# Kernel optimization log

Hardware: AMD Instinct MI355X
Metric: run time of the kernel (lower is better)

Reference implementation:

```python
import jax, jax.numpy as jnp
import numpy as np

NS, BS, U, NR, NT, D = 256, 7, 8, 4, 8, 2
ITERS, HID = 3, 200
P, NOISE = 100.0, 1e-7
CIN = 2 * NT * D  # block input width: flattened Z1 and Z2


def setup_inputs() -> dict:
    key = jax.random.key(0)
    ks = jax.random.split(key, 21)
    rn = lambda k, s: jax.random.normal(k, s, dtype=jnp.float32)
    inp = {
        'H_re': rn(ks[0], (NS, BS, BS, U, NR, NT)),
        'H_im': rn(ks[1], (NS, BS, BS, U, NR, NT)),
        'V_re': rn(ks[2], (NS, BS, U, NT, D)),
        'V_im': rn(ks[3], (NS, BS, U, NT, D)),
        'w': jnp.ones((U,), jnp.float32),
        'W1_re': rn(ks[4], (ITERS, HID, CIN)) * 0.05,
        'W1_im': rn(ks[5], (ITERS, HID, CIN)) * 0.05,
        'b1_re': rn(ks[6], (ITERS, HID)) * 0.05,
        'b1_im': rn(ks[7], (ITERS, HID)) * 0.05,
        'W2_re': rn(ks[8], (ITERS, HID, HID)) * 0.05,
        'W2_im': rn(ks[9], (ITERS, HID, HID)) * 0.05,
        'b2_re': rn(ks[10], (ITERS, HID)) * 0.05,
        'b2_im': rn(ks[11], (ITERS, HID)) * 0.05,
        'W3_re': rn(ks[12], (ITERS, HID, HID)) * 0.05,
        'W3_im': rn(ks[13], (ITERS, HID, HID)) * 0.05,
        'b3_re': rn(ks[14], (ITERS, HID)) * 0.05,
        'b3_im': rn(ks[15], (ITERS, HID)) * 0.05,
        'W4_re': rn(ks[16], (ITERS, 1, HID)) * 0.05,
        'W4_im': rn(ks[17], (ITERS, 1, HID)) * 0.05,
        'b4_re': rn(ks[18], (ITERS, 1)) * 0.05,
        'b4_im': rn(ks[19], (ITERS, 1)) * 0.05,
    }
    return inp


def _crelu(x):
    # ComplexReLU: relu on real part, imaginary part passes through
    return jax.nn.relu(x.real) + 1j * x.imag


def _clin(x, W, b):
    # torch Linear with complex weights: x @ W.T + b
    return jnp.einsum('...i,oi->...o', x, W) + b


def _iteration(H, V, w, p):
    n = H.shape[0]
    Z = V
    # HV[n,k,l,i,j] = H[n,k,l,i] @ V[n,k,j]  -> [n,BS,BS,U,U,NR,D]
    HV = jnp.einsum('nklirt,nkjtd->nklijrd', H, V)
    ab = jnp.arange(BS)
    au = jnp.arange(U)
    HV2 = HV[:, ab, ab][:, :, au, au]  # HV[:,k,k,i,i] -> [n,BS,U,NR,D]
    # T[n,k,l,i,j] = HV @ HV^H -> [n,BS,BS,U,U,NR,NR]
    T = jnp.einsum('nklijrd,nklijsd->nklijrs', HV, HV.conj())
    I_r = jnp.eye(NR, dtype=HV.dtype)
    # U[n,l,u] = noise*I + sum_{k,j} T[n,k,l,u,j]
    Usum = NOISE * I_r + T.sum(axis=(1, 4))  # [n,BS,U,NR,NR]
    Y = jnp.linalg.solve(Usum, HV2)
    Td = T[:, ab, ab][:, :, au, au]  # T[:,l,l,u,u]
    F = Usum - Td
    Gamma = jnp.einsum('nlurd,nlure->nlude', HV2.conj(), jnp.linalg.solve(F, HV2))
    IG = jnp.eye(D, dtype=HV.dtype) + Gamma  # [n,BS,U,D,D]
    # A[n,l,m,u] = H[n,l,m,u].mH @ Y[n,m,u] -> [n,BS,BS,U,NT,D]
    A = jnp.einsum('nlmurt,nmurd->nlmutd', H.conj(), Y)
    # L[n,l,u] = sum_m A @ IG[m,u] @ A^H -> [n,BS,U,NT,NT]
    L = jnp.einsum('nlmutd,nmude,nlmuse->nluts', A, IG, A.conj())
    All = A[:, ab, ab]  # A[:,l,l] -> [n,BS,U,NT,D]
    Lam = jnp.einsum('nlutd,nlude->nlute', All, IG)
    wv = w.astype(HV.dtype)[None, None, :, None, None]
    Lam = Lam * wv
    L = L * wv
    Z2 = Lam - jnp.einsum('nluts,nlusd->nlutd', L, Z)
    inp = jnp.concatenate([Z.reshape(n, BS, U, NT * D), Z2.reshape(n, BS, U, NT * D)], -1)
    W1, b1, W2, b2, W3, b3, W4, b4 = p
    h = _crelu(_clin(inp, W1, b1))
    h = _crelu(_clin(h, W2, b2))
    h = _crelu(_clin(h, W3, b3))
    step = _clin(h, W4, b4).real  # [n,BS,U,1]
    Vn = Z + step[..., None] * Z2
    fro = (jnp.abs(Vn) ** 2).sum((-2, -1)).sum(2)  # [n,BS]
    scale = jnp.where(fro > P, jnp.sqrt(P / fro), 1.0)
    return Vn * scale[:, :, None, None, None].astype(Vn.dtype)


def reference(H_re, H_im, V_re, V_im, w, W1_re, W1_im, b1_re, b1_im, W2_re, W2_im, b2_re, b2_im, W3_re, W3_im, b3_re, b3_im, W4_re, W4_im, b4_re, b4_im):
    H = (H_re + 1j * H_im).astype(jnp.complex64)
    V = (V_re + 1j * V_im).astype(jnp.complex64)
    # init_input power normalization per (sample, BS)
    fro0 = (jnp.abs(V) ** 2).sum((-2, -1)).sum(2)
    V = V * jnp.sqrt(P / fro0)[:, :, None, None, None].astype(V.dtype)
    c64 = jnp.complex64
    Ws = [(W1_re + 1j * W1_im).astype(c64), (b1_re + 1j * b1_im).astype(c64),
          (W2_re + 1j * W2_im).astype(c64), (b2_re + 1j * b2_im).astype(c64),
          (W3_re + 1j * W3_im).astype(c64), (b3_re + 1j * b3_im).astype(c64),
          (W4_re + 1j * W4_im).astype(c64), (b4_re + 1j * b4_im).astype(c64)]
    for it in range(ITERS):
        p = tuple(a[it] for a in Ws)
        V = _iteration(H, V, w, p)
    return jnp.stack([V.real, V.imag], axis=-1)
```

## Files before the change

kernel.cpp:

```cpp
#include <hip/hip_runtime.h>
#include <math.h>

#define NS 256
#define BS 7
#define UU 8
#define NR 4
#define NT 8
#define DD 2
#define HID 200
#define CIN 32
#define PP 100.0f
#define NOISEF 1e-7f

typedef _Float16 f16x8 __attribute__((ext_vector_type(8)));
typedef float f32x4 __attribute__((ext_vector_type(4)));

#define AST 424
#define AST0 104
#define NTILES 28
#define B1_KC 3
#define B23_KC 13
#define B1_HALVES (B1_KC*NTILES*64*8)
#define B23_HALVES (B23_KC*NTILES*64*8)
#define BITER_HALVES (B1_HALVES + 2*B23_HALVES)
#define MROWS 32

__device__ void chol_solve(const float2 (*A)[NR], const float2 (*B)[DD], float2 (*X)[DD]) {
  float2 L[NR][NR];
  for (int j = 0; j < NR; ++j) {
    float d = A[j][j].x;
    for (int k = 0; k < j; ++k) d -= L[j][k].x * L[j][k].x + L[j][k].y * L[j][k].y;
    float ld = sqrtf(fmaxf(d, 1e-30f));
    L[j][j] = make_float2(ld, 0.f);
    float inv = 1.f / ld;
    for (int i = j + 1; i < NR; ++i) {
      float sr = A[i][j].x, si = A[i][j].y;
      for (int k = 0; k < j; ++k) {
        float2 a = L[i][k], b = L[j][k];
        sr -= a.x * b.x + a.y * b.y;
        si -= a.y * b.x - a.x * b.y;
      }
      L[i][j] = make_float2(sr * inv, si * inv);
    }
  }
  for (int c = 0; c < DD; ++c) {
    float2 z[NR];
    for (int i = 0; i < NR; ++i) {
      float sr = B[i][c].x, si = B[i][c].y;
      for (int k = 0; k < i; ++k) {
        float2 a = L[i][k], zz = z[k];
        sr -= a.x * zz.x - a.y * zz.y;
        si -= a.x * zz.y + a.y * zz.x;
      }
      float inv = 1.f / L[i][i].x;
      z[i] = make_float2(sr * inv, si * inv);
    }
    for (int i = NR - 1; i >= 0; --i) {
      float sr = z[i].x, si = z[i].y;
      for (int k = i + 1; k < NR; ++k) {
        float2 a = L[k][i], xx = X[k][c];
        sr -= a.x * xx.x + a.y * xx.y;
        si -= a.x * xx.y - a.y * xx.x;
      }
      float inv = 1.f / L[i][i].x;
      X[i][c] = make_float2(sr * inv, si * inv);
    }
  }
}

__global__ void k_norm0(const float* __restrict__ Vre, const float* __restrict__ Vim,
                        float2* __restrict__ Vcur) {
  int nl = blockIdx.x;
  int tid = threadIdx.x;
  size_t base = (size_t)nl * 128;
  float re = Vre[base + tid], im = Vim[base + tid];
  float p = re * re + im * im;
  p += __shfl_down(p, 32); p += __shfl_down(p, 16); p += __shfl_down(p, 8);
  p += __shfl_down(p, 4);  p += __shfl_down(p, 2);  p += __shfl_down(p, 1);
  __shared__ float sred[2];
  if ((tid & 63) == 0) sred[tid >> 6] = p;
  __syncthreads();
  float fro = sred[0] + sred[1];
  float sc = sqrtf(PP / fro);
  Vcur[base + tid] = make_float2(re * sc, im * sc);
}

__global__ __launch_bounds__(512, 2) void k_s1n(const float* __restrict__ Hre,
    const float* __restrict__ Him, const float2* __restrict__ Vcur,
    float2* __restrict__ Yb, float2* __restrict__ IGb) {
  int n = blockIdx.x;
  int tid = threadIdx.x;
  int wave = tid >> 6;
  int lane = tid & 63;
  int i = lane >> 3, c = lane & 7;

  __shared__ float2 Vs[952];
  __shared__ float2 Cs[7][76];
  __shared__ float2 Hl[7][268];
  __shared__ float2 Gk[7][8][10];
  __shared__ float2 Gs[56][10];
  __shared__ float2 TdL[56][10];
  __shared__ float2 HV2L[56][8];

  const float2* Vn = Vcur + (size_t)n * 896;
  for (int idx = tid; idx < 896; idx += 512)
    Vs[(idx >> 4) * 17 + (idx & 15)] = Vn[idx];
  __syncthreads();

  if (tid < 448) {
    int k = tid >> 6, e = tid & 63, cc = e >> 3, t = e & 7;
    float sr = 0.f, si = 0.f;
    #pragma unroll
    for (int j = 0; j < 8; ++j) {
      const float2* vr = &Vs[(k * 8 + j) * 17];
      #pragma unroll
      for (int d = 0; d < 2; ++d) {
        float2 a = vr[t * 2 + d], b = vr[cc * 2 + d];
        sr += a.x * b.x + a.y * b.y;
        si += a.y * b.x - a.x * b.y;
      }
    }
    Cs[k][cc * 9 + t] = make_float2(sr, si);
  }

  for (int l = 0; l < BS; ++l) {
    __syncthreads();
    if (tid < 448) {
      int k = tid >> 6;
      int e4 = (tid & 63) * 4;
      size_t hbase = (((size_t)(n * 7 + k) * 7) + l) * 256 + e4;
      float4 re = *(const float4*)(Hre + hbase);
      float4 im = *(const float4*)(Him + hbase);
      int ii = e4 >> 5, rem = e4 & 31;
      float2* hp = &Hl[k][ii * 33 + rem];
      hp[0] = make_float2(re.x, im.x);
      hp[1] = make_float2(re.y, im.y);
      hp[2] = make_float2(re.z, im.z);
      hp[3] = make_float2(re.w, im.w);
    }
    __syncthreads();

    if (wave < 7) {
      int k = wave;
      const float2* hme = &Hl[k][i * 33];
      const float2* cme = &Cs[k][c * 9];
      float2 T[4];
      #pragma unroll
      for (int r = 0; r < 4; ++r) {
        float tr = 0.f, ti = 0.f;
        #pragma unroll
        for (int t = 0; t < 8; ++t) {
          float2 h = hme[r * 8 + t], cv = cme[t];
          tr += h.x * cv.x - h.y * cv.y;
          ti += h.x * cv.y + h.y * cv.x;
        }
        T[r] = make_float2(tr, ti);
      }
      float2 hb[4];
      #pragma unroll
      for (int s = 0; s < 4; ++s) hb[s] = hme[s * 8 + c];
      float2 G[10];
      {
        int ui = 0;
        #pragma unroll
        for (int r = 0; r < 4; ++r)
          #pragma unroll
          for (int s = r; s < 4; ++s) {
            G[ui].x = T[r].x * hb[s].x + T[r].y * hb[s].y;
            G[ui].y = T[r].y * hb[s].x - T[r].x * hb[s].y;
            ++ui;
          }
      }
      #pragma unroll
      for (int m = 1; m < 8; m <<= 1) {
        #pragma unroll
        for (int q = 0; q < 10; ++q) {
          G[q].x += __shfl_xor(G[q].x, m);
          G[q].y += __shfl_xor(G[q].y, m);
        }
      }
      if (c == 0) {
        #pragma unroll
        for (int q = 0; q < 10; ++q) Gk[k][i][q] = G[q];
      }

      if (k == l) {
        int r = c >> 1, d = c & 1;
        float hvx = 0.f, hvy = 0.f;
        const float2* vp = &Vs[(l * 8 + i) * 17 + d];
        #pragma unroll
        for (int t = 0; t < 8; ++t) {
          float2 h = hme[r * 8 + t], v = vp[t * 2];
          hvx += h.x * v.x - h.y * v.y;
          hvy += h.x * v.y + h.y * v.x;
        }
        float gx[8], gy[8];
        int base = lane & 56;
        #pragma unroll
        for (int p = 0; p < 8; ++p) {
          gx[p] = __shfl(hvx, base + p);
          gy[p] = __shfl(hvy, base + p);
        }
        if (c == 0) {
          int ui = 0;
          #pragma unroll
          for (int r2 = 0; r2 < 4; ++r2)
            #pragma unroll
            for (int s2 = r2; s2 < 4; ++s2) {
              float tr = 0.f, ti = 0.f;
              #pragma unroll
              for (int d2 = 0; d2 < 2; ++d2) {
                float ax = gx[r2 * 2 + d2], ay = gy[r2 * 2 + d2];
                float bx = gx[s2 * 2 + d2], by = gy[s2 * 2 + d2];
                tr += ax * bx + ay * by;
                ti += ay * bx - ax * by;
              }
              TdL[l * 8 + i][ui] = make_float2(tr, ti);
              ++ui;
            }
          #pragma unroll
          for (int x = 0; x < 8; ++x)
            HV2L[l * 8 + i][x] = make_float2(gx[x], gy[x]);
        }
      }
    }
    __syncthreads();
    if (tid < 80) {
      int ii = tid / 10, q = tid % 10;
      float sx = 0.f, sy = 0.f;
      #pragma unroll
      for (int k = 0; k < 7; ++k) {
        float2 g = Gk[k][ii][q];
        sx += g.x; sy += g.y;
      }
      Gs[l * 8 + ii][q] = make_float2(sx, sy);
    }
  }
  __syncthreads();

  if (tid < 128) {
    int which = tid >> 6;
    int b = tid & 63;
    if (b < 56) {
      float2 M[NR][NR];
      int ui = 0;
      #pragma unroll
      for (int r = 0; r < 4; ++r)
        #pragma unroll
        for (int s = r; s < 4; ++s) {
          float2 g = Gs[b][ui];
          if (which) { float2 td = TdL[b][ui]; g.x -= td.x; g.y -= td.y; }
          ++ui;
          M[r][s] = g;
          M[s][r] = make_float2(g.x, -g.y);
        }
      #pragma unroll
      for (int r = 0; r < 4; ++r) { M[r][r].x += NOISEF; M[r][r].y = 0.f; }
      float2 Bv[NR][DD], X[NR][DD];
      #pragma unroll
      for (int x = 0; x < 8; ++x) Bv[x >> 1][x & 1] = HV2L[b][x];
      chol_solve(M, Bv, X);
      size_t gb = (size_t)n * 56 + b;
      if (!which) {
        #pragma unroll
        for (int x = 0; x < 8; ++x) Yb[gb * 8 + x] = X[x >> 1][x & 1];
      } else {
        #pragma unroll
        for (int d = 0; d < DD; ++d)
          #pragma unroll
          for (int e = 0; e < DD; ++e) {
            float gr = (d == e) ? 1.f : 0.f, gi = 0.f;
            #pragma unroll
            for (int r = 0; r < NR; ++r) {
              float2 a = Bv[r][d], x = X[r][e];
              gr += a.x * x.x + a.y * x.y;
              gi += a.x * x.y - a.y * x.x;
            }
            IGb[gb * 4 + d * 2 + e] = make_float2(gr, gi);
          }
      }
    }
  }
}

__global__ __launch_bounds__(256) void k_stage2(const float* __restrict__ Hre,
    const float* __restrict__ Him, const float2* __restrict__ Vcur,
    const float2* __restrict__ Yb, const float2* __restrict__ IGb,
    const float* __restrict__ w, float2* __restrict__ Z2out) {
  int nl = blockIdx.x; int l = nl % BS; int n = nl / BS;
  int tid = threadIdx.x;
  __shared__ float2 SM[3686];
  float2* Hsm  = SM;
  float2* Bsm  = SM;
  float2* Lsm  = SM + 952;
  float2* Ysm  = SM + 1792;
  float2* IGsm = SM + 2247;
  float2* Asm  = SM + 2478;
  float2* Lamm = SM + 3430;
  float2* Zlm  = SM + 3558;

  size_t hbase = ((size_t)n * BS + l) * 1792;
  for (int idx = tid; idx < 1792; idx += 256) {
    int t = idx & 7, r = (idx >> 3) & 3, u = (idx >> 5) & 7, m = idx >> 8;
    Hsm[((u * 4 + r) * 7 + m) * 8 + t] = make_float2(Hre[hbase + idx], Him[hbase + idx]);
  }
  const float2* yp = Yb + (size_t)n * 448;
  for (int idx = tid; idx < 448; idx += 256)
    Ysm[(idx >> 6) * 65 + (idx & 63)] = yp[idx];
  const float2* igp = IGb + (size_t)n * 224;
  if (tid < 224) IGsm[(tid >> 5) * 33 + (tid & 31)] = igp[tid];
  const float2* zp = Vcur + (size_t)nl * 128;
  if (tid < 128) Zlm[tid] = zp[tid];
  __syncthreads();

  for (int idx = tid; idx < 896; idx += 256) {
    int u = idx / 112, rem = idx % 112, m = rem >> 4, t = (rem >> 1) & 7, d = rem & 1;
    float ar = 0.f, ai = 0.f;
    #pragma unroll
    for (int r = 0; r < NR; ++r) {
      float2 h = Hsm[((u * 4 + r) * 7 + m) * 8 + t];
      float2 y = Ysm[m * 65 + u * 8 + r * 2 + d];
      ar += h.x * y.x + h.y * y.y;
      ai += h.x * y.y - h.y * y.x;
    }
    Asm[u * 119 + m * 17 + t * 2 + d] = make_float2(ar, ai);
  }
  __syncthreads();

  for (int idx = tid; idx < 896; idx += 256) {
    int u = idx / 112, rem = idx % 112, m = rem >> 4, t = (rem >> 1) & 7, e = rem & 1;
    float br = 0.f, bi = 0.f;
    #pragma unroll
    for (int d = 0; d < DD; ++d) {
      float2 a = Asm[u * 119 + m * 17 + t * 2 + d];
      float2 g = IGsm[m * 33 + u * 4 + d * 2 + e];
      br += a.x * g.x - a.y * g.y;
      bi += a.x * g.y + a.y * g.x;
    }
    Bsm[u * 119 + m * 17 + t * 2 + e] = make_float2(br, bi);
  }
  __syncthreads();

  for (int idx = tid; idx < 512; idx += 256) {
    int u = idx >> 6, t = (idx >> 3) & 7, s = idx & 7;
    float lr = 0.f, li = 0.f;
    #pragma unroll
    for (int m = 0; m < BS; ++m)
      #pragma unroll
      for (int e = 0; e < DD; ++e) {
        float2 bb = Bsm[u * 119 + m * 17 + t * 2 + e];
        float2 ac = Asm[u * 119 + m * 17 + s * 2 + e];
        lr += bb.x * ac.x + bb.y * ac.y;
        li += bb.y * ac.x - bb.x * ac.y;
      }
    float wu = w[u];
    Lsm[(u * 8 + t) * 8 + s] = make_float2(lr * wu, li * wu);
  }
  if (tid < 128) {
    int u = tid >> 4, t = (tid >> 1) & 7, e = tid & 1;
    float ar = 0.f, ai = 0.f;
    #pragma unroll
    for (int d = 0; d < DD; ++d) {
      float2 a = Asm[u * 119 + l * 17 + t * 2 + d];
      float2 g = IGsm[l * 33 + u * 4 + d * 2 + e];
      ar += a.x * g.x - a.y * g.y;
      ai += a.x * g.y + a.y * g.x;
    }
    float wu = w[u];
    Lamm[u * 16 + t * 2 + e] = make_float2(ar * wu, ai * wu);
  }
  __syncthreads();

  if (tid < 128) {
    int u = tid >> 4, t = (tid >> 1) & 7, d = tid & 1;
    float2 lam = Lamm[u * 16 + t * 2 + d];
    float zr = lam.x, zi = lam.y;
    #pragma unroll
    for (int s = 0; s < NT; ++s) {
      float2 Lts = Lsm[(u * 8 + t) * 8 + s];
      float2 z = Zlm[u * 16 + s * 2 + d];
      zr -= Lts.x * z.x - Lts.y * z.y;
      zi -= Lts.x * z.y + Lts.y * z.x;
    }
    Z2out[(size_t)nl * 128 + u * 16 + t * 2 + d] = make_float2(zr, zi);
  }
}

__global__ __launch_bounds__(256) void k_pack(
    const float* __restrict__ W1re, const float* __restrict__ W1im,
    const float* __restrict__ b1re, const float* __restrict__ b1im,
    const float* __restrict__ W2re, const float* __restrict__ W2im,
    const float* __restrict__ b2re, const float* __restrict__ b2im,
    const float* __restrict__ W3re, const float* __restrict__ W3im,
    const float* __restrict__ b3re, const float* __restrict__ b3im,
    _Float16* __restrict__ Bout) {
  int gid = blockIdx.x * 256 + threadIdx.x;
  int lane = gid & 63;
  int rest = gid >> 6;
  int nt = rest % NTILES;
  int id2 = rest / NTILES;
  if (id2 >= 87) return;
  int iter = id2 / 29, kk = id2 % 29;
  int layer, kc;
  if (kk < 3)       { layer = 0; kc = kk; }
  else if (kk < 16) { layer = 1; kc = kk - 3; }
  else              { layer = 2; kc = kk - 16; }
  const float *Wr, *Wi, *br, *bi;
  if (layer == 0) { Wr = W1re + iter*HID*CIN; Wi = W1im + iter*HID*CIN; br = b1re + iter*HID; bi = b1im + iter*HID; }
  else if (layer == 1) { Wr = W2re + iter*HID*HID; Wi = W2im + iter*HID*HID; br = b2re + iter*HID; bi = b2im + iter*HID; }
  else { Wr = W3re + iter*HID*HID; Wi = W3im + iter*HID*HID; br = b3re + iter*HID; bi = b3im + iter*HID; }
  int c = nt * 16 + (lane & 15);
  int o = c >> 1; int odd = c & 1;
  f16x8 frag;
  #pragma unroll
  for (int j = 0; j < 8; ++j) {
    int k = kc * 32 + (lane >> 4) * 8 + j;
    float v = 0.f;
    if (o < HID) {
      if (layer == 0) {
        if (k < 32)       v = odd ? Wi[o*32 + k] : Wr[o*32 + k];
        else if (k < 64)  { int i = k - 32; v = odd ? Wr[o*32 + i] : -Wi[o*32 + i]; }
        else if (k == 64) v = odd ? bi[o] : br[o];
      } else {
        if (k < 200)       v = odd ? Wi[o*200 + k] : Wr[o*200 + k];
        else if (k == 207) v = odd ? bi[o] : br[o];
        else if (k >= 208 && k < 408) { int i = k - 208; v = odd ? Wr[o*200 + i] : -Wi[o*200 + i]; }
      }
    }
    frag[j] = (_Float16)v;
  }
  size_t off = (size_t)iter * BITER_HALVES
             + (layer == 0 ? 0 : (layer == 1 ? B1_HALVES : (B1_HALVES + B23_HALVES)))
             + ((size_t)(kc * NTILES + nt) * 64 + lane) * 8;
  *(f16x8*)(Bout + off) = frag;
}

template<int ASTRIDE, int KC, int NTL>
__device__ inline void do_gemm(const _Float16* Ain,
                               const _Float16* __restrict__ Bg,
                               _Float16* Aout, int tbase, int lane) {
  f32x4 acc[2][NTL];
  #pragma unroll
  for (int rt = 0; rt < 2; ++rt)
    #pragma unroll
    for (int nt = 0; nt < NTL; ++nt)
      acc[rt][nt] = (f32x4){0.f, 0.f, 0.f, 0.f};
  const int r0 = lane & 15, g = lane >> 4;
  const _Float16* bp0 = Bg + ((size_t)tbase * 64 + lane) * 8;
  const size_t KSTEP = (size_t)NTILES * 512;
  #pragma unroll
  for (int kc = 0; kc < KC; ++kc) {
    f16x8 b[NTL], a[2];
    #pragma unroll
    for (int nt = 0; nt < NTL; ++nt)
      b[nt] = *(const f16x8*)(bp0 + (size_t)kc * KSTEP + nt * 512);
    #pragma unroll
    for (int rt = 0; rt < 2; ++rt)
      a[rt] = *(const f16x8*)(Ain + (r0 + rt * 16) * ASTRIDE + kc * 32 + 8 * g);
    #pragma unroll
    for (int nt = 0; nt < NTL; ++nt)
      #pragma unroll
      for (int rt = 0; rt < 2; ++rt)
        acc[rt][nt] = __builtin_amdgcn_mfma_f32_16x16x32_f16(a[rt], b[nt], acc[rt][nt], 0, 0, 0);
  }
  #pragma unroll
  for (int nt = 0; nt < NTL; ++nt) {
    int c = (tbase + nt) * 16 + r0;
    int o = c >> 1;
    bool isre = !(c & 1);
    if (o < HID) {
      _Float16* outp = Aout + (isre ? o : 208 + o);
      #pragma unroll
      for (int rt = 0; rt < 2; ++rt)
        #pragma unroll
        for (int q = 0; q < 4; ++q) {
          float v = acc[rt][nt][q];
          if (isre) v = fmaxf(v, 0.f);
          outp[(size_t)(rt * 16 + g * 4 + q) * AST] = (_Float16)v;
        }
    }
  }
}

__global__ __launch_bounds__(512, 2) void k_mlp_mfma(
    const float2* __restrict__ Vcur, const float2* __restrict__ Z2,
    const _Float16* __restrict__ Bp,
    const float* __restrict__ W4re, const float* __restrict__ W4im,
    const float* __restrict__ b4re,
    float2* __restrict__ Vout) {
  int b = blockIdx.x;
  int tid = threadIdx.x;
  int wave = tid >> 6, lane = tid & 63;
  int tb = (wave < 4) ? wave * 4 : 16 + (wave - 4) * 3;

  __shared__ _Float16 A0[MROWS * AST0];
  __shared__ _Float16 Abuf[2][MROWS * AST];
  __shared__ float2 Zs[MROWS][16];
  __shared__ float2 Z2s[MROWS][16];
  __shared__ float w4s[2][HID];
  __shared__ float stepv[MROWS];
  __shared__ float scs[4];

  for (int idx = tid; idx < MROWS * 16; idx += 512) {
    ((float2*)Zs)[idx]  = Vcur[(size_t)b * (MROWS * 16) + idx];
    ((float2*)Z2s)[idx] = Z2[(size_t)b * (MROWS * 16) + idx];
  }
  for (int idx = tid; idx < HID; idx += 512) {
    w4s[0][idx] = W4re[idx];
    w4s[1][idx] = W4im[idx];
  }
  __syncthreads();

  for (int idx = tid; idx < MROWS * AST0; idx += 512) {
    int m = idx / AST0, c = idx % AST0;
    float v;
    if (c < 64) {
      int f = c & 31;
      float2 z = (f < 16) ? Zs[m][f] : Z2s[m][f - 16];
      v = (c >= 32) ? z.y : z.x;
    } else v = (c == 64) ? 1.f : 0.f;
    A0[m * AST0 + c] = (_Float16)v;
  }
  for (int idx = tid; idx < 2 * MROWS * 16; idx += 512) {
    int buf = idx >> 9, rem = idx & 511, m = rem >> 4, p = rem & 15;
    int c = (p < 8) ? (200 + p) : (400 + p);
    Abuf[buf][m * AST + c] = (p == 7) ? (_Float16)1.f : (_Float16)0.f;
  }
  __syncthreads();

  if (wave < 4) do_gemm<AST0, B1_KC, 4>(A0, Bp, &Abuf[0][0], tb, lane);
  else          do_gemm<AST0, B1_KC, 3>(A0, Bp, &Abuf[0][0], tb, lane);
  __syncthreads();
  if (wave < 4) do_gemm<AST, B23_KC, 4>(&Abuf[0][0], Bp + B1_HALVES, &Abuf[1][0], tb, lane);
  else          do_gemm<AST, B23_KC, 3>(&Abuf[0][0], Bp + B1_HALVES, &Abuf[1][0], tb, lane);
  __syncthreads();
  if (wave < 4) do_gemm<AST, B23_KC, 4>(&Abuf[1][0], Bp + B1_HALVES + B23_HALVES, &Abuf[0][0], tb, lane);
  else          do_gemm<AST, B23_KC, 3>(&Abuf[1][0], Bp + B1_HALVES + B23_HALVES, &Abuf[0][0], tb, lane);
  __syncthreads();

  {
    int m = tid >> 4, q = tid & 15;
    float acc = 0.f;
    for (int o = q; o < HID; o += 16) {
      float hr = (float)Abuf[0][m * AST + o];
      float hi = (float)Abuf[0][m * AST + 208 + o];
      acc += hr * w4s[0][o] - hi * w4s[1][o];
    }
    acc += __shfl_down(acc, 8, 16);
    acc += __shfl_down(acc, 4, 16);
    acc += __shfl_down(acc, 2, 16);
    acc += __shfl_down(acc, 1, 16);
    if (q == 0) stepv[m] = acc + b4re[0];
  }
  __syncthreads();

  {
    int idx = tid;
    int m = idx >> 4, f = idx & 15;
    float st = stepv[m];
    float2 z = Zs[m][f], z2 = Z2s[m][f];
    Zs[m][f] = make_float2(fmaf(st, z2.x, z.x), fmaf(st, z2.y, z.y));
  }
  __syncthreads();

  if (wave < 4) {
    const float2* vp = &Zs[wave * 8][0];
    float2 v0 = vp[lane * 2], v1 = vp[lane * 2 + 1];
    float p = v0.x * v0.x + v0.y * v0.y + v1.x * v1.x + v1.y * v1.y;
    p += __shfl_down(p, 32); p += __shfl_down(p, 16); p += __shfl_down(p, 8);
    p += __shfl_down(p, 4);  p += __shfl_down(p, 2);  p += __shfl_down(p, 1);
    if (lane == 0) scs[wave] = (p > PP) ? sqrtf(PP / p) : 1.f;
  }
  __syncthreads();
  {
    int idx = tid;
    float sc = scs[idx >> 7];
    float2 v = ((float2*)Zs)[idx];
    Vout[(size_t)b * (MROWS * 16) + idx] = make_float2(v.x * sc, v.y * sc);
  }
}

extern "C" void kernel_launch(void* const* d_in, const int* in_sizes, int n_in,
                              void* d_out, int out_size, void* d_ws, size_t ws_size,
                              hipStream_t stream) {
  const float* Hre  = (const float*)d_in[0];
  const float* Him  = (const float*)d_in[1];
  const float* Vre  = (const float*)d_in[2];
  const float* Vim  = (const float*)d_in[3];
  const float* w    = (const float*)d_in[4];
  const float* W1re = (const float*)d_in[5];
  const float* W1im = (const float*)d_in[6];
  const float* b1re = (const float*)d_in[7];
  const float* b1im = (const float*)d_in[8];
  const float* W2re = (const float*)d_in[9];
  const float* W2im = (const float*)d_in[10];
  const float* b2re = (const float*)d_in[11];
  const float* b2im = (const float*)d_in[12];
  const float* W3re = (const float*)d_in[13];
  const float* W3im = (const float*)d_in[14];
  const float* b3re = (const float*)d_in[15];
  const float* b3im = (const float*)d_in[16];
  const float* W4re = (const float*)d_in[17];
  const float* W4im = (const float*)d_in[18];
  const float* b4re = (const float*)d_in[19];

  const size_t NV = (size_t)NS * BS * UU * NT * DD;
  const size_t NB = (size_t)NS * BS * UU;
  float2* Vcur = (float2*)d_ws;
  float2* Z2b  = Vcur + NV;
  float2* Yb   = Z2b + NV;
  float2* IGb  = Yb + NB * 8;
  _Float16* Bpack = (_Float16*)(IGb + NB * 4);

  k_pack<<<609, 256, 0, stream>>>(W1re, W1im, b1re, b1im, W2re, W2im, b2re, b2im,
                                  W3re, W3im, b3re, b3im, Bpack);
  k_norm0<<<NS * BS, 128, 0, stream>>>(Vre, Vim, Vcur);
  for (int it = 0; it < 3; ++it) {
    k_s1n<<<NS, 512, 0, stream>>>(Hre, Him, Vcur, Yb, IGb);
    k_stage2<<<NS * BS, 256, 0, stream>>>(Hre, Him, Vcur, Yb, IGb, w, Z2b);
    float2* vout = (it == 2) ? (float2*)d_out : Vcur;
    k_mlp_mfma<<<NS * BS * UU * NT * DD / (MROWS * 16), 512, 0, stream>>>(Vcur, Z2b,
        Bpack + (size_t)it * BITER_HALVES,
        W4re + it * HID, W4im + it * HID, b4re + it, vout);
  }
}
```

Before: 218.9 us.

## Fuse stage-1 solve and stage-2 Z2 computation into a single per-sample kernel

Merges the per-sample Cholesky/solve kernel with the per-(sample,BS) Z2 kernel so Y and IG stay in shared memory instead of going through global workspace, and removes one launch per iteration. The stage-2 work now loops serially over the 7 BS indices inside each of 256 blocks, reusing an aliased shared buffer. This trades global traffic and launch overhead for much lower grid parallelism and more block-level barriers.

```diff
diff --git a/kernel.cpp b/kernel.cpp
--- a/kernel.cpp
+++ b/kernel.cpp
@@ -85,22 +85,31 @@
   Vcur[base + tid] = make_float2(re * sc, im * sc);
 }
 
-__global__ __launch_bounds__(512, 2) void k_s1n(const float* __restrict__ Hre,
+__global__ __launch_bounds__(512, 2) void k_s1s2(const float* __restrict__ Hre,
     const float* __restrict__ Him, const float2* __restrict__ Vcur,
-    float2* __restrict__ Yb, float2* __restrict__ IGb) {
+    const float* __restrict__ w, float2* __restrict__ Z2out) {
   int n = blockIdx.x;
   int tid = threadIdx.x;
   int wave = tid >> 6;
   int lane = tid & 63;
   int i = lane >> 3, c = lane & 7;
 
-  __shared__ float2 Vs[952];
-  __shared__ float2 Cs[7][76];
-  __shared__ float2 Hl[7][268];
-  __shared__ float2 Gk[7][8][10];
-  __shared__ float2 Gs[56][10];
-  __shared__ float2 TdL[56][10];
-  __shared__ float2 HV2L[56][8];
+  __shared__ float2 SM[6160];
+  float2* Vs   = SM;
+  float2* YL   = SM + 952;
+  float2* IGL  = SM + 1400;
+  float2* R    = SM + 1624;
+  float2* Cs   = R;
+  float2* Hl   = R + 532;
+  float2* Gk   = R + 2408;
+  float2* Gs   = R + 2968;
+  float2* TdL  = R + 3528;
+  float2* HV2L = R + 4088;
+  float2* Hsm  = R;
+  float2* Bsm  = R;
+  float2* Asm  = R + 2408;
+  float2* Lsm  = R + 3360;
+  float2* Lamm = R + 3872;
 
   const float2* Vn = Vcur + (size_t)n * 896;
   for (int idx = tid; idx < 896; idx += 512)
@@ -120,7 +129,7 @@
         si += a.y * b.x - a.x * b.y;
       }
     }
-    Cs[k][cc * 9 + t] = make_float2(sr, si);
+    Cs[k * 76 + cc * 9 + t] = make_float2(sr, si);
   }
 
   for (int l = 0; l < BS; ++l) {
@@ -132,7 +141,7 @@
       float4 re = *(const float4*)(Hre + hbase);
       float4 im = *(const float4*)(Him + hbase);
       int ii = e4 >> 5, rem = e4 & 31;
-      float2* hp = &Hl[k][ii * 33 + rem];
+      float2* hp = &Hl[k * 268 + ii * 33 + rem];
       hp[0] = make_float2(re.x, im.x);
       hp[1] = make_float2(re.y, im.y);
       hp[2] = make_float2(re.z, im.z);
@@ -142,8 +151,8 @@
 
     if (wave < 7) {
       int k = wave;
-      const float2* hme = &Hl[k][i * 33];
-      const float2* cme = &Cs[k][c * 9];
+      const float2* hme = &Hl[k * 268 + i * 33];
+      const float2* cme = &Cs[k * 76 + c * 9];
       float2 T[4];
       #pragma unroll
       for (int r = 0; r < 4; ++r) {
@@ -181,7 +190,7 @@
       }
       if (c == 0) {
         #pragma unroll
-        for (int q = 0; q < 10; ++q) Gk[k][i][q] = G[q];
+        for (int q = 0; q < 10; ++q) Gk[(k * 8 + i) * 10 + q] = G[q];
       }
 
       if (k == l) {
@@ -215,12 +224,12 @@
                 tr += ax * bx + ay * by;
                 ti += ay * bx - ax * by;
               }
-              TdL[l * 8 + i][ui] = make_float2(tr, ti);
+              TdL[(l * 8 + i) * 10 + ui] = make_float2(tr, ti);
               ++ui;
             }
           #pragma unroll
           for (int x = 0; x < 8; ++x)
-            HV2L[l * 8 + i][x] = make_float2(gx[x], gy[x]);
+            HV2L[(l * 8 + i) * 8 + x] = make_float2(gx[x], gy[x]);
         }
       }
     }
@@ -230,10 +239,10 @@
       float sx = 0.f, sy = 0.f;
       #pragma unroll
       for (int k = 0; k < 7; ++k) {
-        float2 g = Gk[k][ii][q];
+        float2 g = Gk[(k * 8 + ii) * 10 + q];
         sx += g.x; sy += g.y;
       }
-      Gs[l * 8 + ii][q] = make_float2(sx, sy);
+      Gs[(l * 8 + ii) * 10 + q] = make_float2(sx, sy);
     }
   }
   __syncthreads();
@@ -248,8 +257,8 @@
       for (int r = 0; r < 4; ++r)
         #pragma unroll
         for (int s = r; s < 4; ++s) {
-          float2 g = Gs[b][ui];
-          if (which) { float2 td = TdL[b][ui]; g.x -= td.x; g.y -= td.y; }
+          float2 g = Gs[b * 10 + ui];
+          if (which) { float2 td = TdL[b * 10 + ui]; g.x -= td.x; g.y -= td.y; }
           ++ui;
           M[r][s] = g;
           M[s][r] = make_float2(g.x, -g.y);
@@ -258,12 +267,11 @@
       for (int r = 0; r < 4; ++r) { M[r][r].x += NOISEF; M[r][r].y = 0.f; }
       float2 Bv[NR][DD], X[NR][DD];
       #pragma unroll
-      for (int x = 0; x < 8; ++x) Bv[x >> 1][x & 1] = HV2L[b][x];
+      for (int x = 0; x < 8; ++x) Bv[x >> 1][x & 1] = HV2L[b * 8 + x];
       chol_solve(M, Bv, X);
-      size_t gb = (size_t)n * 56 + b;
       if (!which) {
         #pragma unroll
-        for (int x = 0; x < 8; ++x) Yb[gb * 8 + x] = X[x >> 1][x & 1];
+        for (int x = 0; x < 8; ++x) YL[b * 8 + x] = X[x >> 1][x & 1];
       } else {
         #pragma unroll
         for (int d = 0; d < DD; ++d)
@@ -276,113 +284,95 @@
               gr += a.x * x.x + a.y * x.y;
               gi += a.x * x.y - a.y * x.x;
             }
-            IGb[gb * 4 + d * 2 + e] = make_float2(gr, gi);
+            IGL[b * 4 + d * 2 + e] = make_float2(gr, gi);
           }
       }
     }
   }
-}
-
-__global__ __launch_bounds__(256) void k_stage2(const float* __restrict__ Hre,
-    const float* __restrict__ Him, const float2* __restrict__ Vcur,
-    const float2* __restrict__ Yb, const float2* __restrict__ IGb,
-    const float* __restrict__ w, float2* __restrict__ Z2out) {
-  int nl = blockIdx.x; int l = nl % BS; int n = nl / BS;
-  int tid = threadIdx.x;
-  __shared__ float2 SM[3686];
-  float2* Hsm  = SM;
-  float2* Bsm  = SM;
-  float2* Lsm  = SM + 952;
-  float2* Ysm  = SM + 1792;
-  float2* IGsm = SM + 2247;
-  float2* Asm  = SM + 2478;
-  float2* Lamm = SM + 3430;
-  float2* Zlm  = SM + 3558;
-
-  size_t hbase = ((size_t)n * BS + l) * 1792;
-  for (int idx = tid; idx < 1792; idx += 256) {
-    int t = idx & 7, r = (idx >> 3) & 3, u = (idx >> 5) & 7, m = idx >> 8;
-    Hsm[((u * 4 + r) * 7 + m) * 8 + t] = make_float2(Hre[hbase + idx], Him[hbase + idx]);
-  }
-  const float2* yp = Yb + (size_t)n * 448;
-  for (int idx = tid; idx < 448; idx += 256)
-    Ysm[(idx >> 6) * 65 + (idx & 63)] = yp[idx];
-  const float2* igp = IGb + (size_t)n * 224;
-  if (tid < 224) IGsm[(tid >> 5) * 33 + (tid & 31)] = igp[tid];
-  const float2* zp = Vcur + (size_t)nl * 128;
-  if (tid < 128) Zlm[tid] = zp[tid];
-  __syncthreads();
-
-  for (int idx = tid; idx < 896; idx += 256) {
-    int u = idx / 112, rem = idx % 112, m = rem >> 4, t = (rem >> 1) & 7, d = rem & 1;
-    float ar = 0.f, ai = 0.f;
-    #pragma unroll
-    for (int r = 0; r < NR; ++r) {
-      float2 h = Hsm[((u * 4 + r) * 7 + m) * 8 + t];
-      float2 y = Ysm[m * 65 + u * 8 + r * 2 + d];
-      ar += h.x * y.x + h.y * y.y;
-      ai += h.x * y.y - h.y * y.x;
-    }
-    Asm[u * 119 + m * 17 + t * 2 + d] = make_float2(ar, ai);
-  }
-  __syncthreads();
-
-  for (int idx = tid; idx < 896; idx += 256) {
-    int u = idx / 112, rem = idx % 112, m = rem >> 4, t = (rem >> 1) & 7, e = rem & 1;
-    float br = 0.f, bi = 0.f;
-    #pragma unroll
-    for (int d = 0; d < DD; ++d) {
-      float2 a = Asm[u * 119 + m * 17 + t * 2 + d];
-      float2 g = IGsm[m * 33 + u * 4 + d * 2 + e];
-      br += a.x * g.x - a.y * g.y;
-      bi += a.x * g.y + a.y * g.x;
-    }
-    Bsm[u * 119 + m * 17 + t * 2 + e] = make_float2(br, bi);
-  }
-  __syncthreads();
-
-  for (int idx = tid; idx < 512; idx += 256) {
-    int u = idx >> 6, t = (idx >> 3) & 7, s = idx & 7;
-    float lr = 0.f, li = 0.f;
-    #pragma unroll
-    for (int m = 0; m < BS; ++m)
-      #pragma unroll
-      for (int e = 0; e < DD; ++e) {
-        float2 bb = Bsm[u * 119 + m * 17 + t * 2 + e];
-        float2 ac = Asm[u * 119 + m * 17 + s * 2 + e];
-        lr += bb.x * ac.x + bb.y * ac.y;
-        li += bb.y * ac.x - bb.x * ac.y;
-      }
-    float wu = w[u];
-    Lsm[(u * 8 + t) * 8 + s] = make_float2(lr * wu, li * wu);
-  }
-  if (tid < 128) {
-    int u = tid >> 4, t = (tid >> 1) & 7, e = tid & 1;
-    float ar = 0.f, ai = 0.f;
-    #pragma unroll
-    for (int d = 0; d < DD; ++d) {
-      float2 a = Asm[u * 119 + l * 17 + t * 2 + d];
-      float2 g = IGsm[l * 33 + u * 4 + d * 2 + e];
-      ar += a.x * g.x - a.y * g.y;
-      ai += a.x * g.y + a.y * g.x;
-    }
-    float wu = w[u];
-    Lamm[u * 16 + t * 2 + e] = make_float2(ar * wu, ai * wu);
-  }
-  __syncthreads();
-
-  if (tid < 128) {
-    int u = tid >> 4, t = (tid >> 1) & 7, d = tid & 1;
-    float2 lam = Lamm[u * 16 + t * 2 + d];
-    float zr = lam.x, zi = lam.y;
-    #pragma unroll
-    for (int s = 0; s < NT; ++s) {
-      float2 Lts = Lsm[(u * 8 + t) * 8 + s];
-      float2 z = Zlm[u * 16 + s * 2 + d];
-      zr -= Lts.x * z.x - Lts.y * z.y;
-      zi -= Lts.x * z.y + Lts.y * z.x;
-    }
-    Z2out[(size_t)nl * 128 + u * 16 + t * 2 + d] = make_float2(zr, zi);
+  __syncthreads();
+
+  for (int l2 = 0; l2 < BS; ++l2) {
+    {
+      size_t hbase = ((size_t)(n * 7 + l2) * 7) * 256;
+      for (int idx = tid; idx < 1792; idx += 512) {
+        int t = idx & 7, r = (idx >> 3) & 3, u = (idx >> 5) & 7, m = idx >> 8;
+        Hsm[((u * 4 + r) * 7 + m) * 8 + t] = make_float2(Hre[hbase + idx], Him[hbase + idx]);
+      }
+    }
+    __syncthreads();
+
+    for (int idx = tid; idx < 896; idx += 512) {
+      int u = idx / 112, rem = idx % 112, m = rem >> 4, t = (rem >> 1) & 7, d = rem & 1;
+      float ar = 0.f, ai = 0.f;
+      #pragma unroll
+      for (int r = 0; r < NR; ++r) {
+        float2 h = Hsm[((u * 4 + r) * 7 + m) * 8 + t];
+        float2 y = YL[(m * 8 + u) * 8 + r * 2 + d];
+        ar += h.x * y.x + h.y * y.y;
+        ai += h.x * y.y - h.y * y.x;
+      }
+      Asm[u * 119 + m * 17 + t * 2 + d] = make_float2(ar, ai);
+    }
+    __syncthreads();
+
+    for (int idx = tid; idx < 896; idx += 512) {
+      int u = idx / 112, rem = idx % 112, m = rem >> 4, t = (rem >> 1) & 7, e = rem & 1;
+      float br = 0.f, bi = 0.f;
+      #pragma unroll
+      for (int d = 0; d < DD; ++d) {
+        float2 a = Asm[u * 119 + m * 17 + t * 2 + d];
+        float2 g = IGL[(m * 8 + u) * 4 + d * 2 + e];
+        br += a.x * g.x - a.y * g.y;
+        bi += a.x * g.y + a.y * g.x;
+      }
+      Bsm[u * 119 + m * 17 + t * 2 + e] = make_float2(br, bi);
+    }
+    __syncthreads();
+
+    if (tid < 512) {
+      int u = tid >> 6, t = (tid >> 3) & 7, s = tid & 7;
+      float lr = 0.f, li = 0.f;
+      #pragma unroll
+      for (int m = 0; m < BS; ++m)
+        #pragma unroll
+        for (int e = 0; e < DD; ++e) {
+          float2 bb = Bsm[u * 119 + m * 17 + t * 2 + e];
+          float2 ac = Asm[u * 119 + m * 17 + s * 2 + e];
+          lr += bb.x * ac.x + bb.y * ac.y;
+          li += bb.y * ac.x - bb.x * ac.y;
+        }
+      float wu = w[u];
+      Lsm[(u * 8 + t) * 8 + s] = make_float2(lr * wu, li * wu);
+    }
+    if (tid < 128) {
+      int u = tid >> 4, t = (tid >> 1) & 7, e = tid & 1;
+      float ar = 0.f, ai = 0.f;
+      #pragma unroll
+      for (int d = 0; d < DD; ++d) {
+        float2 a = Asm[u * 119 + l2 * 17 + t * 2 + d];
+        float2 g = IGL[(l2 * 8 + u) * 4 + d * 2 + e];
+        ar += a.x * g.x - a.y * g.y;
+        ai += a.x * g.y + a.y * g.x;
+      }
+      float wu = w[u];
+      Lamm[u * 16 + t * 2 + e] = make_float2(ar * wu, ai * wu);
+    }
+    __syncthreads();
+
+    if (tid < 128) {
+      int u = tid >> 4, t = (tid >> 1) & 7, d = tid & 1;
+      float2 lam = Lamm[u * 16 + t * 2 + d];
+      float zr = lam.x, zi = lam.y;
+      #pragma unroll
+      for (int s = 0; s < NT; ++s) {
+        float2 Lts = Lsm[(u * 8 + t) * 8 + s];
+        float2 z = Vs[(l2 * 8 + u) * 17 + s * 2 + d];
+        zr -= Lts.x * z.x - Lts.y * z.y;
+        zi -= Lts.x * z.y + Lts.y * z.x;
+      }
+      Z2out[((size_t)(n * 7 + l2)) * 128 + u * 16 + t * 2 + d] = make_float2(zr, zi);
+    }
+    __syncthreads();
   }
 }
 
@@ -605,19 +595,15 @@
   const float* b4re = (const float*)d_in[19];
 
   const size_t NV = (size_t)NS * BS * UU * NT * DD;
-  const size_t NB = (size_t)NS * BS * UU;
   float2* Vcur = (float2*)d_ws;
   float2* Z2b  = Vcur + NV;
-  float2* Yb   = Z2b + NV;
-  float2* IGb  = Yb + NB * 8;
-  _Float16* Bpack = (_Float16*)(IGb + NB * 4);
+  _Float16* Bpack = (_Float16*)(Z2b + NV);
 
   k_pack<<<609, 256, 0, stream>>>(W1re, W1im, b1re, b1im, W2re, W2im, b2re, b2im,
                                   W3re, W3im, b3re, b3im, Bpack);
   k_norm0<<<NS * BS, 128, 0, stream>>>(Vre, Vim, Vcur);
   for (int it = 0; it < 3; ++it) {
-    k_s1n<<<NS, 512, 0, stream>>>(Hre, Him, Vcur, Yb, IGb);
-    k_stage2<<<NS * BS, 256, 0, stream>>>(Hre, Him, Vcur, Yb, IGb, w, Z2b);
+    k_s1s2<<<NS, 512, 0, stream>>>(Hre, Him, Vcur, w, Z2b);
     float2* vout = (it == 2) ? (float2*)d_out : Vcur;
     k_mlp_mfma<<<NS * BS * UU * NT * DD / (MROWS * 16), 512, 0, stream>>>(Vcur, Z2b,
         Bpack + (size_t)it * BITER_HALVES,
```

New measurement: 222.2 us. Within noise of the previous version (+1.5%).
